# Kernel optimization log

Measured on AMD Instinct MI355X. Metric: run time of the kernel, lower is better.

Reference implementation:

```python
import jax, jax.numpy as jnp
import numpy as np

N_STEPS = 5
STATE_DIM = 512
ANN_DIM = 256
N_NODES = 2048
N_EDGE_TYPES = 4


def setup_inputs() -> dict:
    key = jax.random.key(0)
    ks = jax.random.split(key, 12)
    D, E, N = STATE_DIM, N_EDGE_TYPES, N_NODES
    s = 0.02
    adjacency = (jax.random.uniform(ks[0], (N, N * 2 * E)) < 0.015).astype(jnp.float32)
    annotations = jax.random.normal(ks[1], (N, ANN_DIM), dtype=jnp.float32)
    W_prop = jax.random.normal(ks[2], (2 * E, D, D), dtype=jnp.float32) * s
    b_prop = jnp.zeros((2 * E, D), dtype=jnp.float32)
    Wz = jax.random.normal(ks[3], (D, D), dtype=jnp.float32) * s
    Uz = jax.random.normal(ks[4], (D, D), dtype=jnp.float32) * s
    bz = jnp.zeros((D,), dtype=jnp.float32)
    Wr = jax.random.normal(ks[5], (D, D), dtype=jnp.float32) * s
    Ur = jax.random.normal(ks[6], (D, D), dtype=jnp.float32) * s
    br = jnp.zeros((D,), dtype=jnp.float32)
    Wh = jax.random.normal(ks[7], (D, D), dtype=jnp.float32) * s
    Uh = jax.random.normal(ks[8], (D, D), dtype=jnp.float32) * s
    bh = jnp.zeros((D,), dtype=jnp.float32)
    return dict(adjacency=adjacency, annotations=annotations, W_prop=W_prop, b_prop=b_prop,
                Wz=Wz, Uz=Uz, bz=bz, Wr=Wr, Ur=Ur, br=br, Wh=Wh, Uh=Uh, bh=bh)


def reference(adjacency, annotations, W_prop, b_prop, Wz, Uz, bz, Wr, Ur, br, Wh, Uh, bh):
    N = annotations.shape[0]
    D = W_prop.shape[-1]
    # pad annotations into first columns of state (input1[:, :ann_dim] = annotations)
    h = jnp.zeros((N, D), dtype=annotations.dtype).at[:, :annotations.shape[1]].set(annotations)
    for _ in range(N_STEPS):
        # per-edge-type linear transforms: edge_type_list [2E, N, D]
        t = jnp.einsum('nd,edf->enf', h, W_prop) + b_prop[:, None, :]
        # adjacency aggregation: A is [N, N*2E] with per-edge-type column blocks
        a = adjacency @ t.reshape(-1, D)  # [N, D]
        # GRU node update (UpdateNet)
        z = jax.nn.sigmoid(a @ Wz + h @ Uz + bz)
        r = jax.nn.sigmoid(a @ Wr + h @ Ur + br)
        h_tilde = jnp.tanh(a @ Wh + (r * h) @ Uh + bh)
        h = (1.0 - z) * h + z * h_tilde
    return h
```

## Files before the change

kernel.cpp:

```cpp
#include <hip/hip_runtime.h>

typedef __attribute__((ext_vector_type(8))) short short8;
typedef __attribute__((ext_vector_type(4))) float floatx4;
typedef __attribute__((ext_vector_type(4))) unsigned uintx4;

#define NSTEPS 5
#define DD 512
#define ANN 256
#define NNODE 2048
#define NEDGE 8
#define NCOLS (NNODE * NEDGE)
#define MAXE 96
#define KP (NEDGE * DD)


typedef __attribute__((address_space(3))) unsigned lds_u32;
typedef const __attribute__((address_space(1))) unsigned g_u32;
__device__ __forceinline__ void gload16(const short* g, short* l) {
    __builtin_amdgcn_global_load_lds((g_u32*)g, (lds_u32*)l, 16, 0, 0);
}

__device__ inline float bf2f(unsigned short s) {
    unsigned u = ((unsigned)s) << 16;
    float f; __builtin_memcpy(&f, &u, 4);
    return f;
}
__device__ inline unsigned short f2bf(float f) {
    unsigned u; __builtin_memcpy(&u, &f, 4);
    u += 0x7fffu + ((u >> 16) & 1u);
    return (unsigned short)(u >> 16);
}
__device__ inline void split2(float x, unsigned short& hi, unsigned short& lo) {
    hi = f2bf(x);
    lo = f2bf(x - bf2f(hi));
}
__device__ inline void fo_write(short* __restrict__ Fhi, short* __restrict__ Flo,
                                int row, int col, float v) {
    unsigned short hs, ls;
    split2(v, hs, ls);
    size_t a = ((size_t)(row >> 4) * 64 + (col >> 3)) * 128 + ((row & 15) << 3) + (col & 7);
    Fhi[a] = (short)hs;
    Flo[a] = (short)ls;
}
__device__ inline void fo_write2(short* __restrict__ Fhi, short* __restrict__ Flo,
                                 int row, int c, float v0, float v1) {
    unsigned short h0, l0, h1, l1;
    split2(v0, h0, l0);
    split2(v1, h1, l1);
    size_t a = ((size_t)(row >> 4) * 64 + (c >> 3)) * 128 + ((row & 15) << 3) + (c & 7);
    *(unsigned*)(Fhi + a) = (unsigned)h0 | ((unsigned)h1 << 16);
    *(unsigned*)(Flo + a) = (unsigned)l0 | ((unsigned)l1 << 16);
}

__global__ __launch_bounds__(256) void k_init(const float* __restrict__ ann,
                                              float* __restrict__ h,
                                              short* __restrict__ HBhi,
                                              short* __restrict__ HBlo,
                                              int* __restrict__ cnt2,
                                              unsigned short* __restrict__ idx) {
    int n = blockIdx.x, t = threadIdx.x;
    int c = 2 * t;
    float v0 = 0.f, v1 = 0.f;
    if (c < ANN) {
        v0 = ann[(size_t)n * ANN + c];
        v1 = ann[(size_t)n * ANN + c + 1];
    }
    h[(size_t)n * DD + c]     = v0;
    h[(size_t)n * DD + c + 1] = v1;
    fo_write2(HBhi, HBlo, n, c, v0, v1);
    if (t < NEDGE) cnt2[n * NEDGE + t] = 0;
    unsigned* ip = (unsigned*)(idx + (size_t)n * NEDGE * MAXE);
    for (int j = t; j < NEDGE * MAXE / 2; j += 256)
        ip[j] = 2048u | (2048u << 16);
    if (n == 0) {
        h[(size_t)NNODE * DD + c]     = 0.f;
        h[(size_t)NNODE * DD + c + 1] = 0.f;
    }
}

__global__ __launch_bounds__(256) void k_build(const float* __restrict__ adj,
                                               int* __restrict__ cnt2,
                                               unsigned short* __restrict__ idx) {
    int n = blockIdx.x;
    const float* row = adj + (size_t)n * NCOLS;
    for (int j8 = threadIdx.x; j8 < NCOLS / 8; j8 += 256) {
        floatx4 a = *(const floatx4*)(row + j8 * 8);
        floatx4 b = *(const floatx4*)(row + j8 * 8 + 4);
        unsigned nz = 0;
        #pragma unroll
        for (int i = 0; i < 4; i++) {
            if (a[i] != 0.f) nz |= 1u << i;
            if (b[i] != 0.f) nz |= 1u << (4 + i);
        }
        while (nz) {
            int i = __builtin_ctz(nz);
            nz &= nz - 1;
            int j = j8 * 8 + i;
            int e = j >> 11;
            int m = j & (NNODE - 1);
            int p = atomicAdd(&cnt2[n * NEDGE + e], 1);
            if (p < MAXE) idx[((size_t)n * NEDGE + e) * MAXE + p] = (unsigned short)m;
        }
    }
}

__global__ __launch_bounds__(256) void k_transP(const float* __restrict__ W,
                                                short* __restrict__ Fhi,
                                                short* __restrict__ Flo, int K) {
    __shared__ float st[32][33];
    int tx = threadIdx.x & 31, ty = threadIdx.x >> 5;
    int k0 = blockIdx.x * 32, n0 = blockIdx.y * 32;
    #pragma unroll
    for (int i = 0; i < 4; i++)
        st[ty + i * 8][tx] = W[(size_t)(k0 + ty + i * 8) * DD + n0 + tx];
    __syncthreads();
    #pragma unroll
    for (int i = 0; i < 4; i++) {
        int n = n0 + ty + i * 8, k = k0 + tx;
        float v = st[tx][ty + i * 8];
        unsigned short hs, ls;
        split2(v, hs, ls);
        size_t a = ((size_t)(n >> 4) * (K >> 3) + (k >> 3)) * 128 + ((n & 15) << 3) + (k & 7);
        Fhi[a] = (short)hs;
        Flo[a] = (short)ls;
    }
}

__global__ __launch_bounds__(256) void k_transG(const float* __restrict__ s00,
                                                const float* __restrict__ s10,
                                                const float* __restrict__ s01,
                                                const float* __restrict__ s11,
                                                short* __restrict__ Fhi,
                                                short* __restrict__ Flo) {
    __shared__ float st[32][33];
    const int K = 2 * DD;
    int tx = threadIdx.x & 31, ty = threadIdx.x >> 5;
    int k0 = blockIdx.x * 32, n0 = blockIdx.y * 32;
    const float* sk0 = (n0 < DD) ? s00 : s01;
    const float* sk1 = (n0 < DD) ? s10 : s11;
    #pragma unroll
    for (int i = 0; i < 4; i++) {
        int k = k0 + ty + i * 8;
        const float* s = (k < DD) ? sk0 : sk1;
        st[ty + i * 8][tx] = s[(size_t)(k & (DD - 1)) * DD + ((n0 + tx) & (DD - 1))];
    }
    __syncthreads();
    #pragma unroll
    for (int i = 0; i < 4; i++) {
        int n = n0 + ty + i * 8, k = k0 + tx;
        float v = st[tx][ty + i * 8];
        unsigned short hs, ls;
        split2(v, hs, ls);
        size_t a = ((size_t)(n >> 4) * (K >> 3) + (k >> 3)) * 128 + ((n & 15) << 3) + (k & 7);
        Fhi[a] = (short)hs;
        Flo[a] = (short)ls;
    }
}

__global__ __launch_bounds__(256) void k_gather_all(const float* __restrict__ h,
                                                    const int* __restrict__ cnt2,
                                                    const unsigned short* __restrict__ idx,
                                                    short* __restrict__ Gbhi,
                                                    short* __restrict__ Gblo) {
    __shared__ unsigned short sidx[4 * MAXE];
    __shared__ int scnt[4];
    const int b = blockIdx.x;
    const int x = b & 7;
    const int u = b >> 3;
    const int n = x * 256 + (u >> 1);
    const int half = u & 1;
    const int t = threadIdx.x;
    const int th = t & 127;
    const int eg = t >> 7;

    if (t < 4) scnt[t] = cnt2[n * NEDGE + half * 4 + t];
    {
        const unsigned* src = (const unsigned*)(idx + ((size_t)n * NEDGE + half * 4) * MAXE);
        if (t < 4 * MAXE / 2) ((unsigned*)sidx)[t] = src[t];
    }
    __syncthreads();

    const float* hp = h + 4 * th;
    size_t wbase = ((size_t)(n >> 4) * 512) * 128 + ((n & 15) << 3) + ((th & 1) << 2);

    #pragma unroll 1
    for (int ee = 0; ee < 2; ee++) {
        const int el = eg * 2 + ee;
        const int ge = half * 4 + el;
        int m = scnt[el];
        m = m > MAXE ? MAXE : m;
        m = (m + 7) & ~7;
        const unsigned short* row = &sidx[el * MAXE];
        floatx4 a0 = (floatx4){0.f, 0.f, 0.f, 0.f};
        floatx4 a1 = (floatx4){0.f, 0.f, 0.f, 0.f};
        for (int i = 0; i < m; i += 8) {
            uintx4 w = *(const uintx4*)(row + i);
            floatx4 v0 = *(const floatx4*)(hp + (size_t)(w[0] & 0xffffu) * DD);
            floatx4 v1 = *(const floatx4*)(hp + (size_t)(w[0] >> 16) * DD);
            floatx4 v2 = *(const floatx4*)(hp + (size_t)(w[1] & 0xffffu) * DD);
            floatx4 v3 = *(const floatx4*)(hp + (size_t)(w[1] >> 16) * DD);
            floatx4 v4 = *(const floatx4*)(hp + (size_t)(w[2] & 0xffffu) * DD);
            floatx4 v5 = *(const floatx4*)(hp + (size_t)(w[2] >> 16) * DD);
            floatx4 v6 = *(const floatx4*)(hp + (size_t)(w[3] & 0xffffu) * DD);
            floatx4 v7 = *(const floatx4*)(hp + (size_t)(w[3] >> 16) * DD);
            a0 += v0; a1 += v1; a0 += v2; a1 += v3;
            a0 += v4; a1 += v5; a0 += v6; a1 += v7;
        }
        floatx4 a = a0 + a1;

        unsigned short hs[4], ls[4];
        #pragma unroll
        for (int j = 0; j < 4; j++) split2(a[j], hs[j], ls[j]);
        unsigned long long hpk = (unsigned long long)hs[0] | ((unsigned long long)hs[1] << 16)
                               | ((unsigned long long)hs[2] << 32) | ((unsigned long long)hs[3] << 48);
        unsigned long long lpk = (unsigned long long)ls[0] | ((unsigned long long)ls[1] << 16)
                               | ((unsigned long long)ls[2] << 32) | ((unsigned long long)ls[3] << 48);
        size_t addr = wbase + (size_t)(ge * 64 + (th >> 1)) * 128;
        __builtin_nontemporal_store(hpk, (unsigned long long*)(Gbhi + addr));
        __builtin_nontemporal_store(lpk, (unsigned long long*)(Gblo + addr));
    }
}

template<int MODE>
__global__ __launch_bounds__(256, 4) void k_gemm8(
    const short* __restrict__ A0hi, const short* __restrict__ A0lo,
    const short* __restrict__ A1hi, const short* __restrict__ A1lo,
    const short* __restrict__ Bhi,  const short* __restrict__ Blo,
    const float* __restrict__ bias0, const float* __restrict__ bias1,
    float* __restrict__ zbuf,
    float* __restrict__ h,
    short* __restrict__ Ohi, short* __restrict__ Olo,
    float* __restrict__ P0, float* __restrict__ P1) {

    __shared__ short S[24][512];

    const int tid = threadIdx.x;
    const int lane = tid & 63;
    const int wave = tid >> 6;
    const int wm = wave >> 1;
    const int wn = wave & 1;
    const int quad = lane >> 4;
    const int l16 = lane & 15;

    const int pbid = blockIdx.x;
    const int x = pbid & 7;
    const int j = pbid >> 3;
    const int mband = x * 4 + (j & 3);
    int kh, bx;
    if (MODE == 1) { kh = 0; bx = j >> 2; }
    else           { kh = (j >> 2) & 1; bx = j >> 3; }
    const int blockM = mband * 64;
    const int blockN = bx * 32;
    const int mt0 = blockM >> 4, nt0 = blockN >> 4;
    const int KCB = (MODE == 0) ? 512 : 128;
    const int bko = (MODE == 0) ? kh * 256 : (MODE == 2 ? kh * 64 : 0);
    const int Kloc = (MODE == 0) ? 2048 : (MODE == 1 ? 1024 : 512);

    const short* Ahi_s = (MODE == 2 && kh) ? A1hi : A0hi;
    const short* Alo_s = (MODE == 2 && kh) ? A1lo : A0lo;

    floatx4 acc[2];
    acc[0] = (floatx4){0.f, 0.f, 0.f, 0.f};
    acc[1] = (floatx4){0.f, 0.f, 0.f, 0.f};

    auto gaddr = [&](int k0, int s) -> const short* {
        if (s < 16) {
            int pl = s >> 3, u = s & 7;
            int mt = u >> 1, ks = u & 1;
            const short* base;
            int kc, stride;
            if (MODE == 0) {
                base = pl ? A0lo : A0hi;
                kc = kh * 256 + (k0 >> 3) + ks * 4;
                stride = 512;
            } else if (MODE == 1) {
                int seg = k0 >> 9;
                base = seg ? (pl ? A1lo : A1hi) : (pl ? A0lo : A0hi);
                kc = ((k0 & 511) >> 3) + ks * 4;
                stride = 64;
            } else {
                base = pl ? Alo_s : Ahi_s;
                kc = (k0 >> 3) + ks * 4;
                stride = 64;
            }
            return base + ((size_t)(mt0 + mt) * stride + kc) * 128;
        } else {
            int u = s - 16, pl = u >> 2, ks = (u >> 1) & 1, nt = u & 1;
            const short* base = pl ? Blo : Bhi;
            return base + ((size_t)(nt0 + nt) * KCB + bko + (k0 >> 3) + ks * 4) * 128;
        }
    };

    for (int k0 = 0; k0 < Kloc; k0 += 64) {
        #pragma unroll
        for (int jj = 0; jj < 6; jj++) {
            int s = jj * 4 + wave;
            gload16(gaddr(k0, s) + lane * 8, &S[s][lane * 8]);
        }
        __syncthreads();

        #pragma unroll
        for (int ks = 0; ks < 2; ks++) {
            short8 ah[2], al[2], bh, bl;
            #pragma unroll
            for (int mi = 0; mi < 2; mi++) {
                ah[mi] = *(const short8*)&S[(wm * 2 + mi) * 2 + ks][lane * 8];
                al[mi] = *(const short8*)&S[8 + (wm * 2 + mi) * 2 + ks][lane * 8];
            }
            bh = *(const short8*)&S[16 + ks * 2 + wn][lane * 8];
            bl = *(const short8*)&S[20 + ks * 2 + wn][lane * 8];
            #pragma unroll
            for (int mi = 0; mi < 2; mi++) {
                acc[mi] = __builtin_amdgcn_mfma_f32_16x16x32_bf16(ah[mi], bh, acc[mi], 0, 0, 0);
                acc[mi] = __builtin_amdgcn_mfma_f32_16x16x32_bf16(ah[mi], bl, acc[mi], 0, 0, 0);
                acc[mi] = __builtin_amdgcn_mfma_f32_16x16x32_bf16(al[mi], bh, acc[mi], 0, 0, 0);
            }
        }
        __syncthreads();
    }

    float* P = kh ? P1 : P0;
    #pragma unroll
    for (int mi = 0; mi < 2; mi++) {
        int gcol = blockN + wn * 16 + l16;
        #pragma unroll
        for (int r = 0; r < 4; r++) {
            int grow = blockM + wm * 32 + mi * 16 + quad * 4 + r;
            float v = acc[mi][r];
            if (MODE == 0 || MODE == 2) {
                P[(size_t)grow * DD + gcol] = v;
            } else {
                if (gcol < DD) {
                    size_t o = (size_t)grow * DD + gcol;
                    zbuf[o] = 1.f / (1.f + __expf(-(v + bias0[gcol])));
                } else {
                    int c = gcol - DD;
                    size_t o = (size_t)grow * DD + c;
                    float rr = 1.f / (1.f + __expf(-(v + bias1[c])));
                    fo_write(Ohi, Olo, grow, c, rr * h[o]);
                }
            }
        }
    }
}

__global__ __launch_bounds__(256) void k_combP(const float* __restrict__ P0,
                                               const float* __restrict__ P1,
                                               const int* __restrict__ cnt2,
                                               const float* __restrict__ bp,
                                               short* __restrict__ Gahi,
                                               short* __restrict__ Galo) {
    int n = blockIdx.x, t = threadIdx.x;
    int c = 2 * t;
    float s0 = 0.f, s1 = 0.f;
    #pragma unroll
    for (int e = 0; e < NEDGE; e++) {
        float ce = (float)cnt2[n * NEDGE + e];
        s0 += ce * bp[e * DD + c];
        s1 += ce * bp[e * DD + c + 1];
    }
    size_t o = (size_t)n * DD + c;
    float v0 = P0[o] + P1[o] + s0;
    float v1 = P0[o + 1] + P1[o + 1] + s1;
    fo_write2(Gahi, Galo, n, c, v0, v1);
}

__global__ __launch_bounds__(256) void k_combF(const float* __restrict__ P0,
                                               const float* __restrict__ P1,
                                               const float* __restrict__ bh,
                                               const float* __restrict__ zbuf,
                                               float* __restrict__ h,
                                               short* __restrict__ HBhi,
                                               short* __restrict__ HBlo,
                                               float* __restrict__ outF) {
    int n = blockIdx.x, t = threadIdx.x;
    int c = 2 * t;
    size_t o = (size_t)n * DD + c;
    float hn0, hn1;
    {
        float v = P0[o] + P1[o] + bh[c];
        hn0 = (1.f - zbuf[o]) * h[o] + zbuf[o] * tanhf(v);
    }
    {
        float v = P0[o + 1] + P1[o + 1] + bh[c + 1];
        hn1 = (1.f - zbuf[o + 1]) * h[o + 1] + zbuf[o + 1] * tanhf(v);
    }
    h[o] = hn0;
    h[o + 1] = hn1;
    fo_write2(HBhi, HBlo, n, c, hn0, hn1);
    outF[o] = hn0;
    outF[o + 1] = hn1;
}

extern "C" void kernel_launch(void* const* d_in, const int* in_sizes, int n_in,
                              void* d_out, int out_size, void* d_ws, size_t ws_size,
                              hipStream_t stream) {
    const float* adj = (const float*)d_in[0];
    const float* ann = (const float*)d_in[1];
    const float* Wp  = (const float*)d_in[2];
    const float* bp  = (const float*)d_in[3];
    const float* Wz  = (const float*)d_in[4];
    const float* Uz  = (const float*)d_in[5];
    const float* bz  = (const float*)d_in[6];
    const float* Wr  = (const float*)d_in[7];
    const float* Ur  = (const float*)d_in[8];
    const float* br  = (const float*)d_in[9];
    const float* Wh  = (const float*)d_in[10];
    const float* Uh  = (const float*)d_in[11];
    const float* bh  = (const float*)d_in[12];

    char* p = (char*)d_ws;
    float* h     = (float*)p; p += (size_t)(NNODE + 1) * DD * 4;
    float* abuf  = (float*)p; p += (size_t)NNODE * DD * 4;
    float* P0    = (float*)p; p += (size_t)NNODE * DD * 4;
    float* P1    = (float*)p; p += (size_t)NNODE * DD * 4;
    short* Gbhi  = (short*)p; p += (size_t)NNODE * KP * 2;
    short* Gblo  = (short*)p; p += (size_t)NNODE * KP * 2;
    short* Gahi  = (short*)p; p += (size_t)NNODE * DD * 2;
    short* Galo  = (short*)p; p += (size_t)NNODE * DD * 2;
    short* HBhi  = (short*)p; p += (size_t)NNODE * DD * 2;
    short* HBlo  = (short*)p; p += (size_t)NNODE * DD * 2;
    short* RHhi  = (short*)p; p += (size_t)NNODE * DD * 2;
    short* RHlo  = (short*)p; p += (size_t)NNODE * DD * 2;
    short* WpThi = (short*)p; p += (size_t)DD * KP * 2;
    short* WpTlo = (short*)p; p += (size_t)DD * KP * 2;
    short* ZRhi  = (short*)p; p += (size_t)(2 * DD) * (2 * DD) * 2;
    short* ZRlo  = (short*)p; p += (size_t)(2 * DD) * (2 * DD) * 2;
    short* HThi  = (short*)p; p += (size_t)DD * (2 * DD) * 2;
    short* HTlo  = (short*)p; p += (size_t)DD * (2 * DD) * 2;
    unsigned short* idx = (unsigned short*)p;
    p += (size_t)NNODE * NEDGE * MAXE * 2;
    int* cnt2 = (int*)p; p += (size_t)NNODE * NEDGE * 4;

    float* outF = (float*)d_out;

    k_init<<<NNODE, 256, 0, stream>>>(ann, h, HBhi, HBlo, cnt2, idx);
    k_build<<<NNODE, 256, 0, stream>>>(adj, cnt2, idx);
    k_transP<<<dim3(KP / 32, DD / 32), 256, 0, stream>>>(Wp, WpThi, WpTlo, KP);
    k_transG<<<dim3(32, 32), 256, 0, stream>>>(Wz, Uz, Wr, Ur, ZRhi, ZRlo);
    k_transG<<<dim3(32, 16), 256, 0, stream>>>(Wh, Uh, Wh, Uh, HThi, HTlo);

    for (int s = 0; s < NSTEPS; s++) {
        k_gather_all<<<2 * NNODE, 256, 0, stream>>>(h, cnt2, idx, Gbhi, Gblo);
        k_gemm8<0><<<1024, 256, 0, stream>>>(Gbhi, Gblo, nullptr, nullptr,
                                             WpThi, WpTlo, nullptr, nullptr,
                                             nullptr, nullptr, nullptr, nullptr, P0, P1);
        k_combP<<<NNODE, 256, 0, stream>>>(P0, P1, cnt2, bp, Gahi, Galo);
        k_gemm8<1><<<1024, 256, 0, stream>>>(Gahi, Galo, HBhi, HBlo,
                                             ZRhi, ZRlo, bz, br,
                                             abuf, h, RHhi, RHlo, nullptr, nullptr);
        k_gemm8<2><<<1024, 256, 0, stream>>>(Gahi, Galo, RHhi, RHlo,
                                             HThi, HTlo, nullptr, nullptr,
                                             nullptr, nullptr, nullptr, nullptr, P0, P1);
        k_combF<<<NNODE, 256, 0, stream>>>(P0, P1, bh, abuf, h, HBhi, HBlo, outF);
    }
}
```

Before: 1.125 ms.

## Restructure gather kernel to process four nodes per block with 8-wide columns

The sparse gather kernel now assigns each block four nodes and two edge types, with each wavefront handling one node and each lane covering 8 contiguous feature columns (two float4 loads per neighbor). Output is written as 16-byte short8 stores instead of 8-byte nontemporal stores, and the grid shrinks from 4096 to 2048 blocks. This aims to widen per-lane memory accesses and store granularity and to cut block overhead. In exchange it gives up the nontemporal store hint and adds an extra barrier.

New measurement: 906.8 us. 1.24x faster.

```diff
diff --git a/kernel.cpp b/kernel.cpp
--- a/kernel.cpp
+++ b/kernel.cpp
@@ -2,7 +2,7 @@
 
 typedef __attribute__((ext_vector_type(8))) short short8;
 typedef __attribute__((ext_vector_type(4))) float floatx4;
-typedef __attribute__((ext_vector_type(4))) unsigned uintx4;
+typedef __attribute__((ext_vector_type(2))) unsigned uintx2;
 
 #define NSTEPS 5
 #define DD 512
@@ -162,62 +162,82 @@
                                                     const unsigned short* __restrict__ idx,
                                                     short* __restrict__ Gbhi,
                                                     short* __restrict__ Gblo) {
-    __shared__ unsigned short sidx[4 * MAXE];
-    __shared__ int scnt[4];
-    const int b = blockIdx.x;
-    const int x = b & 7;
-    const int u = b >> 3;
-    const int n = x * 256 + (u >> 1);
-    const int half = u & 1;
-    const int t = threadIdx.x;
-    const int th = t & 127;
-    const int eg = t >> 7;
-
-    if (t < 4) scnt[t] = cnt2[n * NEDGE + half * 4 + t];
+    __shared__ unsigned short sidx[8 * MAXE];
+    __shared__ int scnt[8];
+    const int bid = blockIdx.x;
+    const int ep = bid & 3;
+    const int g  = bid >> 2;
+    const int n0 = g * 4;
+    const int t  = threadIdx.x;
+    const int dn = t >> 6;
+    const int th2 = t & 63;
+
+    if (t < 8) scnt[t] = cnt2[(n0 + (t >> 1)) * NEDGE + 2 * ep + (t & 1)];
     {
-        const unsigned* src = (const unsigned*)(idx + ((size_t)n * NEDGE + half * 4) * MAXE);
-        if (t < 4 * MAXE / 2) ((unsigned*)sidx)[t] = src[t];
+        const unsigned* src0 = (const unsigned*)(idx + ((size_t)n0 * NEDGE + 2 * ep) * MAXE);
+        for (int j = t; j < 384; j += 256) {
+            int d = j / 96;
+            int w = j - d * 96;
+            ((unsigned*)sidx)[d * 96 + w] = src0[(size_t)d * (NEDGE * MAXE / 2) + w];
+        }
     }
     __syncthreads();
 
-    const float* hp = h + 4 * th;
-    size_t wbase = ((size_t)(n >> 4) * 512) * 128 + ((n & 15) << 3) + ((th & 1) << 2);
-
-    #pragma unroll 1
-    for (int ee = 0; ee < 2; ee++) {
-        const int el = eg * 2 + ee;
-        const int ge = half * 4 + el;
-        int m = scnt[el];
+    const float* hp = h + 8 * th2;
+
+    floatx4 e0c0, e0c1, e1c0, e1c1;
+    auto gather_edge = [&](int le, floatx4& o0, floatx4& o1) {
+        int m = scnt[dn * 2 + le];
         m = m > MAXE ? MAXE : m;
-        m = (m + 7) & ~7;
-        const unsigned short* row = &sidx[el * MAXE];
+        m = (m + 3) & ~3;
+        const unsigned short* row = &sidx[dn * 192 + le * 96];
         floatx4 a0 = (floatx4){0.f, 0.f, 0.f, 0.f};
         floatx4 a1 = (floatx4){0.f, 0.f, 0.f, 0.f};
-        for (int i = 0; i < m; i += 8) {
-            uintx4 w = *(const uintx4*)(row + i);
-            floatx4 v0 = *(const floatx4*)(hp + (size_t)(w[0] & 0xffffu) * DD);
-            floatx4 v1 = *(const floatx4*)(hp + (size_t)(w[0] >> 16) * DD);
-            floatx4 v2 = *(const floatx4*)(hp + (size_t)(w[1] & 0xffffu) * DD);
-            floatx4 v3 = *(const floatx4*)(hp + (size_t)(w[1] >> 16) * DD);
-            floatx4 v4 = *(const floatx4*)(hp + (size_t)(w[2] & 0xffffu) * DD);
-            floatx4 v5 = *(const floatx4*)(hp + (size_t)(w[2] >> 16) * DD);
-            floatx4 v6 = *(const floatx4*)(hp + (size_t)(w[3] & 0xffffu) * DD);
-            floatx4 v7 = *(const floatx4*)(hp + (size_t)(w[3] >> 16) * DD);
-            a0 += v0; a1 += v1; a0 += v2; a1 += v3;
-            a0 += v4; a1 += v5; a0 += v6; a1 += v7;
-        }
-        floatx4 a = a0 + a1;
-
-        unsigned short hs[4], ls[4];
-        #pragma unroll
-        for (int j = 0; j < 4; j++) split2(a[j], hs[j], ls[j]);
-        unsigned long long hpk = (unsigned long long)hs[0] | ((unsigned long long)hs[1] << 16)
-                               | ((unsigned long long)hs[2] << 32) | ((unsigned long long)hs[3] << 48);
-        unsigned long long lpk = (unsigned long long)ls[0] | ((unsigned long long)ls[1] << 16)
-                               | ((unsigned long long)ls[2] << 32) | ((unsigned long long)ls[3] << 48);
-        size_t addr = wbase + (size_t)(ge * 64 + (th >> 1)) * 128;
-        __builtin_nontemporal_store(hpk, (unsigned long long*)(Gbhi + addr));
-        __builtin_nontemporal_store(lpk, (unsigned long long*)(Gblo + addr));
+        floatx4 b0 = (floatx4){0.f, 0.f, 0.f, 0.f};
+        floatx4 b1 = (floatx4){0.f, 0.f, 0.f, 0.f};
+        for (int i = 0; i < m; i += 4) {
+            uintx2 w = *(const uintx2*)(row + i);
+            const float* r0 = hp + (size_t)(w[0] & 0xffffu) * DD;
+            const float* r1 = hp + (size_t)(w[0] >> 16) * DD;
+            const float* r2 = hp + (size_t)(w[1] & 0xffffu) * DD;
+            const float* r3 = hp + (size_t)(w[1] >> 16) * DD;
+            floatx4 v0 = *(const floatx4*)r0;
+            floatx4 v1 = *(const floatx4*)(r0 + 4);
+            floatx4 v2 = *(const floatx4*)r1;
+            floatx4 v3 = *(const floatx4*)(r1 + 4);
+            floatx4 v4 = *(const floatx4*)r2;
+            floatx4 v5 = *(const floatx4*)(r2 + 4);
+            floatx4 v6 = *(const floatx4*)r3;
+            floatx4 v7 = *(const floatx4*)(r3 + 4);
+            a0 += v0; a1 += v1; b0 += v2; b1 += v3;
+            a0 += v4; a1 += v5; b0 += v6; b1 += v7;
+        }
+        o0 = a0 + b0;
+        o1 = a1 + b1;
+    };
+    gather_edge(0, e0c0, e0c1);
+    gather_edge(1, e1c0, e1c1);
+
+    __syncthreads();
+
+    #pragma unroll
+    for (int le = 0; le < 2; le++) {
+        floatx4 c0 = le ? e1c0 : e0c0;
+        floatx4 c1 = le ? e1c1 : e0c1;
+        int ge = 2 * ep + le;
+        unsigned short hs[8], ls[8];
+        #pragma unroll
+        for (int j = 0; j < 4; j++) {
+            split2(c0[j], hs[j], ls[j]);
+            split2(c1[j], hs[4 + j], ls[4 + j]);
+        }
+        short8 hv, lv;
+        #pragma unroll
+        for (int j = 0; j < 8; j++) { hv[j] = (short)hs[j]; lv[j] = (short)ls[j]; }
+        size_t a = ((size_t)(n0 >> 4) * 512 + ge * 64 + th2) * 128
+                 + (size_t)((n0 & 15) + dn) * 8;
+        *(short8*)(Gbhi + a) = hv;
+        *(short8*)(Gblo + a) = lv;
     }
 }
 
@@ -441,7 +461,7 @@
     k_transG<<<dim3(32, 16), 256, 0, stream>>>(Wh, Uh, Wh, Uh, HThi, HTlo);
 
     for (int s = 0; s < NSTEPS; s++) {
-        k_gather_all<<<2 * NNODE, 256, 0, stream>>>(h, cnt2, idx, Gbhi, Gblo);
+        k_gather_all<<<2048, 256, 0, stream>>>(h, cnt2, idx, Gbhi, Gblo);
         k_gemm8<0><<<1024, 256, 0, stream>>>(Gbhi, Gblo, nullptr, nullptr,
                                              WpThi, WpTlo, nullptr, nullptr,
                                              nullptr, nullptr, nullptr, nullptr, P0, P1);
```
